# Performance work log

Hardware: AMD Instinct MI355X
Metric: run time of the kernel (lower is better)

The kernel has to match this reference:

```python
import jax, jax.numpy as jnp
import numpy as np

B, C, H, W, K = 16, 512, 64, 64, 64  # K = external-attention latent dim (self.k = 64)


def setup_inputs() -> dict:
    key = jax.random.key(0)
    ks = jax.random.split(key, 5)
    x = jax.random.normal(ks[0], (B, C, H, W), dtype=jnp.float32)
    # conv1: Conv2d(c, c, 1) with bias; init normal(0, sqrt(2/(1*1*out_channels)))
    conv1_w = jax.random.normal(ks[1], (C, C), dtype=jnp.float32) * np.float32(np.sqrt(2.0 / C))
    conv1_b = jnp.zeros((C,), dtype=jnp.float32)
    # linear_0: Conv1d(c, k, 1, bias=False); init normal(0, sqrt(2/out_channels))
    lin0_w = jax.random.normal(ks[2], (K, C), dtype=jnp.float32) * np.float32(np.sqrt(2.0 / K))
    # linear_1: Conv1d(k, c, 1, bias=False)
    lin1_w = jax.random.normal(ks[3], (C, K), dtype=jnp.float32) * np.float32(np.sqrt(2.0 / C))
    # conv2: Conv2d(c, c, 1, bias=False)
    conv2_w = jax.random.normal(ks[4], (C, C), dtype=jnp.float32) * np.float32(np.sqrt(2.0 / C))
    return {"x": x, "conv1_w": conv1_w, "conv1_b": conv1_b,
            "lin0_w": lin0_w, "lin1_w": lin1_w, "conv2_w": conv2_w}


def reference(x, conv1_w, conv1_b, lin0_w, lin1_w, conv2_w):
    b, c, h, w = x.shape
    n = h * w
    idn = x
    # conv1: 1x1 conv == per-pixel GEMM
    y = jnp.einsum('oc,bchw->bohw', conv1_w, x) + conv1_b[None, :, None, None]
    y = y.reshape(b, c, n)
    # external attention: linear_0 -> softmax over tokens -> L1 renorm over latent dim
    attn = jnp.einsum('kc,bcn->bkn', lin0_w, y)          # (b, K, n)
    attn = jax.nn.softmax(attn, axis=-1)
    attn = attn / (1e-9 + attn.sum(axis=1, keepdims=True))
    y = jnp.einsum('ck,bkn->bcn', lin1_w, attn)          # (b, c, n)
    # rank: view(-1, c) row-major (as torch .view does), per-row topk threshold,
    # scale below-threshold by 0.75 and the rest by 1.25; output is detached
    # (torch.tensor(pred, requires_grad=False)) -> stop_gradient
    top_k = c // 2
    flat = y.reshape(-1, c)                               # (b*n, c) row-major chunks
    thr = jax.lax.top_k(flat, top_k)[0][:, -1:]           # k-th largest per row
    scaled = jnp.where(flat < thr, 0.75 * flat, 1.25 * flat)
    yr = jax.lax.stop_gradient(scaled).reshape(b, c, h, w)
    # conv2: 1x1 conv no bias + ReLU, residual add, final ReLU
    out = jax.nn.relu(jnp.einsum('oc,bchw->bohw', conv2_w, yr))
    return jax.nn.relu(out + idn)
```

## Files before the change

kernel.cpp:

```cpp
#include <hip/hip_runtime.h>
#include <stdint.h>

typedef unsigned short u16;
typedef unsigned int u32;
using short8 = __attribute__((ext_vector_type(8))) short;
using f32x4  = __attribute__((ext_vector_type(4))) float;

#define BDIM 16
#define CDIM 512
#define KLAT 64
#define NTOK 4096

__device__ __forceinline__ u16 f2bf(float x) {
  union { float f; u32 u; } a; a.f = x;
  u32 r = a.u + 0x7FFFu + ((a.u >> 16) & 1u);
  return (u16)(r >> 16);
}
__device__ __forceinline__ u32 pack2(float a, float b) {
  return (u32)f2bf(a) | ((u32)f2bf(b) << 16);
}
__device__ __forceinline__ u32 f2key(float x) {
  u32 u = __float_as_uint(x);
  return (u & 0x80000000u) ? ~u : (u | 0x80000000u);
}
__device__ __forceinline__ float keyscale(u32 k_, u32 thr) {
  u32 u = (k_ & 0x80000000u) ? (k_ & 0x7FFFFFFFu) : ~k_;
  float v = __uint_as_float(u);
  return (k_ < thr) ? 0.75f * v : 1.25f * v;
}

__global__ __launch_bounds__(256) void k_setup(
    const float* __restrict__ conv1_w, const float* __restrict__ conv1_b,
    const float* __restrict__ lin0_w,  const float* __restrict__ lin1_w,
    const float* __restrict__ conv2_w,
    u16* __restrict__ w0bf, float* __restrict__ b0,
    u16* __restrict__ lin1bf, u16* __restrict__ cwbf)
{
  const int bid = blockIdx.x;
  const int t = threadIdx.x;
  if (bid < 128) {
    const int kb = bid & 15, cb = bid >> 4;
    const int lane = t & 63;
    int k = kb * 4 + (t >> 6);
    k = __builtin_amdgcn_readfirstlane(k);
    const int c = cb * 64 + lane;
    float acc = 0.f;
    const float* l0 = lin0_w + (size_t)k * CDIM;
    const float* cw = conv1_w + c;
#pragma unroll 4
    for (int o = 0; o < CDIM; ++o)
      acc = fmaf(l0[o], cw[(size_t)o * CDIM], acc);
    w0bf[k * CDIM + c] = f2bf(acc);
  } else if (bid == 128) {
    if (t < KLAT) {
      float acc = 0.f;
      for (int c = 0; c < CDIM; ++c) acc = fmaf(lin0_w[t * CDIM + c], conv1_b[c], acc);
      b0[t] = acc;
    }
  } else if (bid < 193) {
    const int b2 = bid - 129;
    const float4* src = (const float4*)conv2_w;
#pragma unroll
    for (int i = 0; i < 4; ++i) {
      int idx = (b2 * 256 + t) + i * 16384;
      float4 v = src[idx];
      uint2 o;
      o.x = pack2(v.x, v.y);
      o.y = pack2(v.z, v.w);
      *(uint2*)(cwbf + (size_t)idx * 4) = o;
    }
  } else {
    const int b2 = bid - 193;
#pragma unroll
    for (int i = 0; i < 4; ++i) {
      int g = b2 * 1024 + i * 256 + t;
      float4 v0 = *(const float4*)(lin1_w + (size_t)g * 8);
      float4 v1 = *(const float4*)(lin1_w + (size_t)g * 8 + 4);
      uint4 o;
      o.x = pack2(v0.x, v0.y); o.y = pack2(v0.z, v0.w);
      o.z = pack2(v1.x, v1.y); o.w = pack2(v1.z, v1.w);
      *(uint4*)(lin1bf + (size_t)g * 8) = o;
    }
  }
}

__global__ __launch_bounds__(256) void k_xpose(
    const float* __restrict__ x, u16* __restrict__ xbt)
{
  __shared__ float tile[32 * 512];
  const int n0 = blockIdx.x * 512, c0 = blockIdx.y * 32, b = blockIdx.z;
  const int t = threadIdx.x;
#pragma unroll
  for (int i = 0; i < 16; ++i) {
    int f4 = t + i * 256;
    int row = f4 >> 7, col4 = f4 & 127;
    float4 v = *(const float4*)(x + ((size_t)(b * CDIM + c0 + row)) * NTOK + n0 + col4 * 4);
    int phys4 = (col4 + row + (row >> 3)) & 127;
    *(float4*)&tile[row * 512 + phys4 * 4] = v;
  }
  __syncthreads();
#pragma unroll
  for (int i = 0; i < 8; ++i) {
    int nr = (t >> 2) + i * 64;
    int cs = (t & 3) * 8;
    float w[8];
#pragma unroll
    for (int j = 0; j < 8; ++j) {
      int row = cs + j;
      int phys4 = ((nr >> 2) + row + (row >> 3)) & 127;
      w[j] = tile[row * 512 + phys4 * 4 + (nr & 3)];
    }
    uint4 o;
    o.x = pack2(w[0], w[1]); o.y = pack2(w[2], w[3]);
    o.z = pack2(w[4], w[5]); o.w = pack2(w[6], w[7]);
    *(uint4*)(xbt + ((size_t)(b * NTOK + n0 + nr)) * CDIM + c0 + cs) = o;
  }
}

__global__ __launch_bounds__(256) void k_logits(
    const u16* __restrict__ w0bf, const u16* __restrict__ xbt,
    const float* __restrict__ b0, float* __restrict__ logits)
{
  __shared__ u16 As[64 * 72];
  __shared__ u16 Bs[128 * 72];
  const int nb = blockIdx.x, b = blockIdx.y;
  const int t = threadIdx.x;
  const int wv = t >> 6, lane = t & 63;
  const int quad = lane >> 4, l15 = lane & 15;
  f32x4 acc[4][2];
#pragma unroll
  for (int mi = 0; mi < 4; ++mi)
#pragma unroll
    for (int ni = 0; ni < 2; ++ni) acc[mi][ni] = (f32x4){0.f, 0.f, 0.f, 0.f};

  for (int kc = 0; kc < 8; ++kc) {
#pragma unroll
    for (int i = 0; i < 2; ++i) {
      int ch = t + i * 256;
      int row = ch >> 3, col = (ch & 7) * 8;
      uint4 a = *(const uint4*)(w0bf + (size_t)row * CDIM + kc * 64 + col);
      *(uint4*)&As[row * 72 + col] = a;
    }
#pragma unroll
    for (int i = 0; i < 4; ++i) {
      int ch = t + i * 256;
      int row = ch >> 3, col = (ch & 7) * 8;
      uint4 bb = *(const uint4*)(xbt + ((size_t)(b * NTOK + nb * 128 + row)) * CDIM + kc * 64 + col);
      *(uint4*)&Bs[row * 72 + col] = bb;
    }
    __syncthreads();
#pragma unroll
    for (int kk = 0; kk < 2; ++kk) {
      short8 af[4], bf_[2];
#pragma unroll
      for (int mi = 0; mi < 4; ++mi)
        af[mi] = *(short8*)&As[(mi * 16 + l15) * 72 + kk * 32 + quad * 8];
#pragma unroll
      for (int ni = 0; ni < 2; ++ni)
        bf_[ni] = *(short8*)&Bs[(wv * 32 + ni * 16 + l15) * 72 + kk * 32 + quad * 8];
#pragma unroll
      for (int mi = 0; mi < 4; ++mi)
#pragma unroll
        for (int ni = 0; ni < 2; ++ni)
          acc[mi][ni] = __builtin_amdgcn_mfma_f32_16x16x32_bf16(
              af[mi], bf_[ni], acc[mi][ni], 0, 0, 0);
    }
    __syncthreads();
  }
#pragma unroll
  for (int mi = 0; mi < 4; ++mi) {
#pragma unroll
    for (int ni = 0; ni < 2; ++ni) {
#pragma unroll
      for (int r = 0; r < 4; ++r) {
        int row = mi * 16 + quad * 4 + r;
        int col = nb * 128 + wv * 32 + ni * 16 + l15;
        logits[((size_t)(b * KLAT + row)) * NTOK + col] = acc[mi][ni][r] + b0[row];
      }
    }
  }
}

__global__ __launch_bounds__(256) void k_softmax(float* __restrict__ attn)
{
  __shared__ float red[4], red2[4];
  const int t = threadIdx.x;
  float* p = attn + (size_t)blockIdx.x * NTOK;
  float4 v[4];
#pragma unroll
  for (int i = 0; i < 4; ++i) v[i] = ((float4*)p)[t + i * 256];
  float m = v[0].x;
#pragma unroll
  for (int i = 0; i < 4; ++i)
    m = fmaxf(m, fmaxf(fmaxf(v[i].x, v[i].y), fmaxf(v[i].z, v[i].w)));
#pragma unroll
  for (int o = 1; o < 64; o <<= 1) m = fmaxf(m, __shfl_xor(m, o));
  const int wv = t >> 6, lane = t & 63;
  if (lane == 0) red[wv] = m;
  __syncthreads();
  m = fmaxf(fmaxf(red[0], red[1]), fmaxf(red[2], red[3]));
  float s = 0.f;
#pragma unroll
  for (int i = 0; i < 4; ++i) {
    v[i].x = __expf(v[i].x - m); s += v[i].x;
    v[i].y = __expf(v[i].y - m); s += v[i].y;
    v[i].z = __expf(v[i].z - m); s += v[i].z;
    v[i].w = __expf(v[i].w - m); s += v[i].w;
  }
#pragma unroll
  for (int o = 1; o < 64; o <<= 1) s += __shfl_xor(s, o);
  if (lane == 0) red2[wv] = s;
  __syncthreads();
  s = red2[0] + red2[1] + red2[2] + red2[3];
  const float inv = 1.f / s;
#pragma unroll
  for (int i = 0; i < 4; ++i) {
    v[i].x *= inv; v[i].y *= inv; v[i].z *= inv; v[i].w *= inv;
    ((float4*)p)[t + i * 256] = v[i];
  }
}

__global__ __launch_bounds__(256) void k_attnT(
    const float* __restrict__ attn, u16* __restrict__ attnT)
{
  __shared__ float tile[64 * 256];
  __shared__ float inv_[256];
  const int n0 = blockIdx.x * 256, b = blockIdx.y;
  const int t = threadIdx.x;
#pragma unroll
  for (int i = 0; i < 16; ++i) {
    int f4 = t + i * 256;
    int row = f4 >> 6, col4 = f4 & 63;
    float4 v = *(const float4*)(attn + ((size_t)(b * KLAT + row)) * NTOK + n0 + col4 * 4);
    int phys4 = (col4 + row + (row >> 3)) & 63;
    *(float4*)&tile[row * 256 + phys4 * 4] = v;
  }
  __syncthreads();
  {
    int n4 = t >> 2, sub = t & 3;
    float s = 0.f;
#pragma unroll
    for (int k = 0; k < 64; ++k) {
      int phys4 = (n4 + k + (k >> 3)) & 63;
      s += tile[k * 256 + phys4 * 4 + sub];
    }
    inv_[t] = 1.f / (1e-9f + s);
  }
  __syncthreads();
#pragma unroll
  for (int i = 0; i < 8; ++i) {
    int nr = (t >> 3) + i * 32;
    int cs = (t & 7) * 8;
    float sc = inv_[nr];
    float w[8];
#pragma unroll
    for (int j = 0; j < 8; ++j) {
      int row = cs + j;
      int phys4 = ((nr >> 2) + row + (row >> 3)) & 63;
      w[j] = tile[row * 256 + phys4 * 4 + (nr & 3)] * sc;
    }
    uint4 o;
    o.x = pack2(w[0], w[1]); o.y = pack2(w[2], w[3]);
    o.z = pack2(w[4], w[5]); o.w = pack2(w[6], w[7]);
    *(uint4*)(attnT + ((size_t)(b * NTOK + n0 + nr)) * KLAT + cs) = o;
  }
}

__global__ __launch_bounds__(256) void k_lin1rank(
    const u16* __restrict__ lin1bf, const u16* __restrict__ attnT,
    u16* __restrict__ yrt)
{
  __shared__ float tile[32 * 512];
  const int n0 = blockIdx.x * 512, c0 = blockIdx.y * 32, b = blockIdx.z;
  const int t = threadIdx.x;
  const int wv = t >> 6, lane = t & 63;
  const int quad = lane >> 4, l15 = lane & 15;

  short8 af[2][2], bfr[8][2];
#pragma unroll
  for (int mi = 0; mi < 2; ++mi)
#pragma unroll
    for (int kk = 0; kk < 2; ++kk)
      af[mi][kk] = *(const short8*)(lin1bf +
          (size_t)(c0 + mi * 16 + l15) * KLAT + kk * 32 + quad * 8);
#pragma unroll
  for (int ni = 0; ni < 8; ++ni)
#pragma unroll
    for (int kk = 0; kk < 2; ++kk)
      bfr[ni][kk] = *(const short8*)(attnT +
          ((size_t)(b * NTOK + n0 + wv * 128 + ni * 16 + l15)) * KLAT + kk * 32 + quad * 8);
  f32x4 acc[2][8];
#pragma unroll
  for (int mi = 0; mi < 2; ++mi)
#pragma unroll
    for (int ni = 0; ni < 8; ++ni) acc[mi][ni] = (f32x4){0.f, 0.f, 0.f, 0.f};
#pragma unroll
  for (int kk = 0; kk < 2; ++kk)
#pragma unroll
    for (int mi = 0; mi < 2; ++mi)
#pragma unroll
      for (int ni = 0; ni < 8; ++ni)
        acc[mi][ni] = __builtin_amdgcn_mfma_f32_16x16x32_bf16(
            af[mi][kk], bfr[ni][kk], acc[mi][ni], 0, 0, 0);
#pragma unroll
  for (int mi = 0; mi < 2; ++mi) {
#pragma unroll
    for (int ni = 0; ni < 8; ++ni) {
#pragma unroll
      for (int r = 0; r < 4; ++r) {
        int row = mi * 16 + quad * 4 + r;
        int col = wv * 128 + ni * 16 + l15;
        int phys4 = ((col >> 2) + row + (row >> 3)) & 127;
        tile[row * 512 + phys4 * 4 + (col & 3)] = acc[mi][ni][r];
      }
    }
  }
  __syncthreads();

  u32 key[8][8];
#pragma unroll
  for (int r = 0; r < 8; ++r) {
    const int row = wv * 8 + r;
    const int rot = row + (row >> 3);
    const int c4a = (lane + rot) & 127;
    const int c4b = (64 + lane + rot) & 127;
    float4 va = *(const float4*)&tile[row * 512 + c4a * 4];
    float4 vb = *(const float4*)&tile[row * 512 + c4b * 4];
    key[r][0] = f2key(va.x); key[r][1] = f2key(va.y);
    key[r][2] = f2key(va.z); key[r][3] = f2key(va.w);
    key[r][4] = f2key(vb.x); key[r][5] = f2key(vb.y);
    key[r][6] = f2key(vb.z); key[r][7] = f2key(vb.w);
  }
  u32 thr[8] = {0u, 0u, 0u, 0u, 0u, 0u, 0u, 0u};
  for (int bit = 31; bit >= 0; --bit) {
    const u32 m = 1u << bit;
#pragma unroll
    for (int r = 0; r < 8; ++r) {
      u32 cand = thr[r] | m;
      int cnt = 0;
#pragma unroll
      for (int j = 0; j < 8; ++j)
        cnt += (int)__popcll(__ballot(key[r][j] >= cand));
      if (cnt >= 256) thr[r] = cand;
    }
  }
#pragma unroll
  for (int r = 0; r < 8; ++r) {
    const int row = wv * 8 + r;
    const int rot = row + (row >> 3);
    const int c4a = (lane + rot) & 127;
    const int c4b = (64 + lane + rot) & 127;
    float4 oa, ob;
    oa.x = keyscale(key[r][0], thr[r]); oa.y = keyscale(key[r][1], thr[r]);
    oa.z = keyscale(key[r][2], thr[r]); oa.w = keyscale(key[r][3], thr[r]);
    ob.x = keyscale(key[r][4], thr[r]); ob.y = keyscale(key[r][5], thr[r]);
    ob.z = keyscale(key[r][6], thr[r]); ob.w = keyscale(key[r][7], thr[r]);
    *(float4*)&tile[row * 512 + c4a * 4] = oa;
    *(float4*)&tile[row * 512 + c4b * 4] = ob;
  }
  __syncthreads();

#pragma unroll
  for (int i = 0; i < 8; ++i) {
    int nr = (t >> 2) + i * 64;
    int cs = (t & 3) * 8;
    float w[8];
#pragma unroll
    for (int j = 0; j < 8; ++j) {
      int row = cs + j;
      int phys4 = ((nr >> 2) + row + (row >> 3)) & 127;
      w[j] = tile[row * 512 + phys4 * 4 + (nr & 3)];
    }
    uint4 o;
    o.x = pack2(w[0], w[1]); o.y = pack2(w[2], w[3]);
    o.z = pack2(w[4], w[5]); o.w = pack2(w[6], w[7]);
    *(uint4*)(yrt + ((size_t)(b * NTOK + n0 + nr)) * CDIM + c0 + cs) = o;
  }
}

__global__ __launch_bounds__(256) void k_conv2(
    const u16* __restrict__ cwbf, const u16* __restrict__ yrt,
    const float* __restrict__ x, float* __restrict__ out)
{
  __shared__ u16 As[128 * 72];
  __shared__ u16 Bs[128 * 72];
  const int nb = blockIdx.x, mb = blockIdx.y, b = blockIdx.z;
  const int t = threadIdx.x;
  const int wv = t >> 6, lane = t & 63;
  const int wm = wv >> 1, wn = wv & 1;
  const int quad = lane >> 4, l15 = lane & 15;
  f32x4 acc[4][4];
#pragma unroll
  for (int mi = 0; mi < 4; ++mi)
#pragma unroll
    for (int ni = 0; ni < 4; ++ni) acc[mi][ni] = (f32x4){0.f, 0.f, 0.f, 0.f};

  for (int kc = 0; kc < 8; ++kc) {
#pragma unroll
    for (int i = 0; i < 4; ++i) {
      int ch = t + i * 256;
      int row = ch >> 3, col = (ch & 7) * 8;
      uint4 a = *(const uint4*)(cwbf + ((size_t)(mb * 128 + row)) * CDIM + kc * 64 + col);
      *(uint4*)&As[row * 72 + col] = a;
      uint4 bb = *(const uint4*)(yrt + ((size_t)(b * NTOK + nb * 128 + row)) * CDIM + kc * 64 + col);
      *(uint4*)&Bs[row * 72 + col] = bb;
    }
    __syncthreads();
#pragma unroll
    for (int kk = 0; kk < 2; ++kk) {
      short8 af[4], bf_[4];
#pragma unroll
      for (int mi = 0; mi < 4; ++mi)
        af[mi] = *(short8*)&As[(wm * 64 + mi * 16 + l15) * 72 + kk * 32 + quad * 8];
#pragma unroll
      for (int ni = 0; ni < 4; ++ni)
        bf_[ni] = *(short8*)&Bs[(wn * 64 + ni * 16 + l15) * 72 + kk * 32 + quad * 8];
#pragma unroll
      for (int mi = 0; mi < 4; ++mi)
#pragma unroll
        for (int ni = 0; ni < 4; ++ni)
          acc[mi][ni] = __builtin_amdgcn_mfma_f32_16x16x32_bf16(
              af[mi], bf_[ni], acc[mi][ni], 0, 0, 0);
    }
    __syncthreads();
  }
#pragma unroll
  for (int mi = 0; mi < 4; ++mi) {
#pragma unroll
    for (int ni = 0; ni < 4; ++ni) {
#pragma unroll
      for (int r = 0; r < 4; ++r) {
        int row = mb * 128 + wm * 64 + mi * 16 + quad * 4 + r;
        int col = nb * 128 + wn * 64 + ni * 16 + l15;
        size_t off = ((size_t)(b * CDIM + row)) * NTOK + col;
        float g = fmaxf(acc[mi][ni][r], 0.f) + x[off];
        out[off] = fmaxf(g, 0.f);
      }
    }
  }
}

extern "C" void kernel_launch(void* const* d_in, const int* in_sizes, int n_in,
                              void* d_out, int out_size, void* d_ws, size_t ws_size,
                              hipStream_t stream)
{
  const float* x       = (const float*)d_in[0];
  const float* conv1_w = (const float*)d_in[1];
  const float* conv1_b = (const float*)d_in[2];
  const float* lin0_w  = (const float*)d_in[3];
  const float* lin1_w  = (const float*)d_in[4];
  const float* conv2_w = (const float*)d_in[5];
  float* out = (float*)d_out;

  char* ws = (char*)d_ws;
  float* attn  = (float*)ws;
  u16*   xbt   = (u16*)(ws + 16777216);
  u16*   yrt   = xbt;
  u16*   attnT = (u16*)d_out;
  char*  wsm   = ws + 16777216 + 67108864;
  u16*   w0bf  = (u16*)wsm;
  float* b0    = (float*)(wsm + 131072);
  u16*   lin1bf= (u16*)(wsm + 131328);
  u16*   cwbf  = (u16*)(wsm + 262400);

  k_setup   <<<197, 256, 0, stream>>>(conv1_w, conv1_b, lin0_w, lin1_w, conv2_w,
                                      w0bf, b0, lin1bf, cwbf);
  k_xpose   <<<dim3(8, 16, 16), 256, 0, stream>>>(x, xbt);
  k_logits  <<<dim3(32, 16), 256, 0, stream>>>(w0bf, xbt, b0, attn);
  k_softmax <<<1024, 256, 0, stream>>>(attn);
  k_attnT   <<<dim3(16, 16), 256, 0, stream>>>(attn, attnT);
  k_lin1rank<<<dim3(8, 16, 16), 256, 0, stream>>>(lin1bf, attnT, yrt);
  k_conv2   <<<dim3(32, 4, 16), 256, 0, stream>>>(cwbf, yrt, x, out);
}
```

Before: 535.9 us.

## Use value-range bisection for per-row top-k threshold and double block threads

The rank kernel now runs 512 threads per block, so each wave owns 4 rows instead of 8 and the matching slices of the MFMA and writeback work. The fixed 32-step radix bit search for the k-th largest key is replaced by a bisection between the row's min and max keys (found with wave shuffles), which stops early when exactly 256 keys reach the midpoint. This is meant to cut the ballot/popcount iterations spent finding the threshold and to raise parallelism. In exchange the loop length now depends on the data and diverges across rows, and each thread holds fewer accumulators.

```diff
diff --git a/kernel.cpp b/kernel.cpp
--- a/kernel.cpp
+++ b/kernel.cpp
@@ -266,7 +266,7 @@
   }
 }
 
-__global__ __launch_bounds__(256) void k_lin1rank(
+__global__ __launch_bounds__(512) void k_lin1rank(
     const u16* __restrict__ lin1bf, const u16* __restrict__ attnT,
     u16* __restrict__ yrt)
 {
@@ -276,7 +276,7 @@
   const int wv = t >> 6, lane = t & 63;
   const int quad = lane >> 4, l15 = lane & 15;
 
-  short8 af[2][2], bfr[8][2];
+  short8 af[2][2], bfr[4][2];
 #pragma unroll
   for (int mi = 0; mi < 2; ++mi)
 #pragma unroll
@@ -284,32 +284,32 @@
       af[mi][kk] = *(const short8*)(lin1bf +
           (size_t)(c0 + mi * 16 + l15) * KLAT + kk * 32 + quad * 8);
 #pragma unroll
-  for (int ni = 0; ni < 8; ++ni)
+  for (int ni = 0; ni < 4; ++ni)
 #pragma unroll
     for (int kk = 0; kk < 2; ++kk)
       bfr[ni][kk] = *(const short8*)(attnT +
-          ((size_t)(b * NTOK + n0 + wv * 128 + ni * 16 + l15)) * KLAT + kk * 32 + quad * 8);
-  f32x4 acc[2][8];
+          ((size_t)(b * NTOK + n0 + wv * 64 + ni * 16 + l15)) * KLAT + kk * 32 + quad * 8);
+  f32x4 acc[2][4];
 #pragma unroll
   for (int mi = 0; mi < 2; ++mi)
 #pragma unroll
-    for (int ni = 0; ni < 8; ++ni) acc[mi][ni] = (f32x4){0.f, 0.f, 0.f, 0.f};
+    for (int ni = 0; ni < 4; ++ni) acc[mi][ni] = (f32x4){0.f, 0.f, 0.f, 0.f};
 #pragma unroll
   for (int kk = 0; kk < 2; ++kk)
 #pragma unroll
     for (int mi = 0; mi < 2; ++mi)
 #pragma unroll
-      for (int ni = 0; ni < 8; ++ni)
+      for (int ni = 0; ni < 4; ++ni)
         acc[mi][ni] = __builtin_amdgcn_mfma_f32_16x16x32_bf16(
             af[mi][kk], bfr[ni][kk], acc[mi][ni], 0, 0, 0);
 #pragma unroll
   for (int mi = 0; mi < 2; ++mi) {
 #pragma unroll
-    for (int ni = 0; ni < 8; ++ni) {
+    for (int ni = 0; ni < 4; ++ni) {
 #pragma unroll
       for (int r = 0; r < 4; ++r) {
         int row = mi * 16 + quad * 4 + r;
-        int col = wv * 128 + ni * 16 + l15;
+        int col = wv * 64 + ni * 16 + l15;
         int phys4 = ((col >> 2) + row + (row >> 3)) & 127;
         tile[row * 512 + phys4 * 4 + (col & 3)] = acc[mi][ni][r];
       }
@@ -317,52 +317,60 @@
   }
   __syncthreads();
 
-  u32 key[8][8];
-#pragma unroll
-  for (int r = 0; r < 8; ++r) {
-    const int row = wv * 8 + r;
+#pragma unroll
+  for (int r = 0; r < 4; ++r) {
+    const int row = wv * 4 + r;
     const int rot = row + (row >> 3);
     const int c4a = (lane + rot) & 127;
     const int c4b = (64 + lane + rot) & 127;
-    float4 va = *(const float4*)&tile[row * 512 + c4a * 4];
-    float4 vb = *(const float4*)&tile[row * 512 + c4b * 4];
-    key[r][0] = f2key(va.x); key[r][1] = f2key(va.y);
-    key[r][2] = f2key(va.z); key[r][3] = f2key(va.w);
-    key[r][4] = f2key(vb.x); key[r][5] = f2key(vb.y);
-    key[r][6] = f2key(vb.z); key[r][7] = f2key(vb.w);
-  }
-  u32 thr[8] = {0u, 0u, 0u, 0u, 0u, 0u, 0u, 0u};
-  for (int bit = 31; bit >= 0; --bit) {
-    const u32 m = 1u << bit;
-#pragma unroll
-    for (int r = 0; r < 8; ++r) {
-      u32 cand = thr[r] | m;
+    float* pa = &tile[row * 512 + c4a * 4];
+    float* pb = &tile[row * 512 + c4b * 4];
+    float4 va = *(const float4*)pa;
+    float4 vb = *(const float4*)pb;
+    u32 key[8];
+    key[0] = f2key(va.x); key[1] = f2key(va.y);
+    key[2] = f2key(va.z); key[3] = f2key(va.w);
+    key[4] = f2key(vb.x); key[5] = f2key(vb.y);
+    key[6] = f2key(vb.z); key[7] = f2key(vb.w);
+    u32 kmin = key[0], kmax = key[0];
+#pragma unroll
+    for (int j = 1; j < 8; ++j) {
+      kmin = key[j] < kmin ? key[j] : kmin;
+      kmax = key[j] > kmax ? key[j] : kmax;
+    }
+#pragma unroll
+    for (int o = 1; o < 64; o <<= 1) {
+      u32 a_ = __shfl_xor(kmin, o), b_ = __shfl_xor(kmax, o);
+      kmin = a_ < kmin ? a_ : kmin;
+      kmax = b_ > kmax ? b_ : kmax;
+    }
+    u32 lo = kmin, hi = kmax;
+    u32 thr;
+    if (lo >= hi) thr = lo;
+    else for (;;) {
+      u32 d = hi - lo;
+      u32 mid = lo + (d >> 1) + (d & 1u);
       int cnt = 0;
 #pragma unroll
       for (int j = 0; j < 8; ++j)
-        cnt += (int)__popcll(__ballot(key[r][j] >= cand));
-      if (cnt >= 256) thr[r] = cand;
-    }
-  }
-#pragma unroll
-  for (int r = 0; r < 8; ++r) {
-    const int row = wv * 8 + r;
-    const int rot = row + (row >> 3);
-    const int c4a = (lane + rot) & 127;
-    const int c4b = (64 + lane + rot) & 127;
+        cnt += (int)__popcll(__ballot(key[j] >= mid));
+      if (cnt == 256) { thr = mid; break; }
+      if (cnt > 256) lo = mid; else hi = mid - 1u;
+      if (lo >= hi) { thr = lo; break; }
+    }
     float4 oa, ob;
-    oa.x = keyscale(key[r][0], thr[r]); oa.y = keyscale(key[r][1], thr[r]);
-    oa.z = keyscale(key[r][2], thr[r]); oa.w = keyscale(key[r][3], thr[r]);
-    ob.x = keyscale(key[r][4], thr[r]); ob.y = keyscale(key[r][5], thr[r]);
-    ob.z = keyscale(key[r][6], thr[r]); ob.w = keyscale(key[r][7], thr[r]);
-    *(float4*)&tile[row * 512 + c4a * 4] = oa;
-    *(float4*)&tile[row * 512 + c4b * 4] = ob;
-  }
-  __syncthreads();
-
-#pragma unroll
-  for (int i = 0; i < 8; ++i) {
-    int nr = (t >> 2) + i * 64;
+    oa.x = keyscale(key[0], thr); oa.y = keyscale(key[1], thr);
+    oa.z = keyscale(key[2], thr); oa.w = keyscale(key[3], thr);
+    ob.x = keyscale(key[4], thr); ob.y = keyscale(key[5], thr);
+    ob.z = keyscale(key[6], thr); ob.w = keyscale(key[7], thr);
+    *(float4*)pa = oa;
+    *(float4*)pb = ob;
+  }
+  __syncthreads();
+
+#pragma unroll
+  for (int i = 0; i < 4; ++i) {
+    int nr = (t >> 2) + i * 128;
     int cs = (t & 3) * 8;
     float w[8];
 #pragma unroll
@@ -469,6 +477,6 @@
   k_logits  <<<dim3(32, 16), 256, 0, stream>>>(w0bf, xbt, b0, attn);
   k_softmax <<<1024, 256, 0, stream>>>(attn);
   k_attnT   <<<dim3(16, 16), 256, 0, stream>>>(attn, attnT);
-  k_lin1rank<<<dim3(8, 16, 16), 256, 0, stream>>>(lin1bf, attnT, yrt);
+  k_lin1rank<<<dim3(8, 16, 16), 512, 0, stream>>>(lin1bf, attnT, yrt);
   k_conv2   <<<dim3(32, 4, 16), 256, 0, stream>>>(cwbf, yrt, x, out);
 }
```

After: 486.3 us. -9.3%, faster.

## Fuse x transpose into logits GEMM, widen rank kernel, range-bisect top-k threshold

Applied to the files above, without the earlier changes.

Removes the standalone transpose/bf16 conversion kernel. The logits GEMM now loads fp32 x directly into a swizzled shared tile and converts to bf16 while building MFMA fragments, which saves a full write and read of the bf16 transposed copy. The lin1+rank kernel moves to 512 threads so each wave handles 4 rows instead of 8. Its per-row k-th-largest search changes from a fixed 32-bit radix walk to a bisection over the row's min..max key range that stops early on an exact count. In exchange there are more LDS reads and conversions inside the GEMM inner loop, and the bisection has a data-dependent iteration count.

```diff
diff --git a/kernel.cpp b/kernel.cpp
--- a/kernel.cpp
+++ b/kernel.cpp
@@ -84,45 +84,12 @@
   }
 }
 
-__global__ __launch_bounds__(256) void k_xpose(
-    const float* __restrict__ x, u16* __restrict__ xbt)
-{
-  __shared__ float tile[32 * 512];
-  const int n0 = blockIdx.x * 512, c0 = blockIdx.y * 32, b = blockIdx.z;
-  const int t = threadIdx.x;
-#pragma unroll
-  for (int i = 0; i < 16; ++i) {
-    int f4 = t + i * 256;
-    int row = f4 >> 7, col4 = f4 & 127;
-    float4 v = *(const float4*)(x + ((size_t)(b * CDIM + c0 + row)) * NTOK + n0 + col4 * 4);
-    int phys4 = (col4 + row + (row >> 3)) & 127;
-    *(float4*)&tile[row * 512 + phys4 * 4] = v;
-  }
-  __syncthreads();
-#pragma unroll
-  for (int i = 0; i < 8; ++i) {
-    int nr = (t >> 2) + i * 64;
-    int cs = (t & 3) * 8;
-    float w[8];
-#pragma unroll
-    for (int j = 0; j < 8; ++j) {
-      int row = cs + j;
-      int phys4 = ((nr >> 2) + row + (row >> 3)) & 127;
-      w[j] = tile[row * 512 + phys4 * 4 + (nr & 3)];
-    }
-    uint4 o;
-    o.x = pack2(w[0], w[1]); o.y = pack2(w[2], w[3]);
-    o.z = pack2(w[4], w[5]); o.w = pack2(w[6], w[7]);
-    *(uint4*)(xbt + ((size_t)(b * NTOK + n0 + nr)) * CDIM + c0 + cs) = o;
-  }
-}
-
 __global__ __launch_bounds__(256) void k_logits(
-    const u16* __restrict__ w0bf, const u16* __restrict__ xbt,
+    const u16* __restrict__ w0bf, const float* __restrict__ x,
     const float* __restrict__ b0, float* __restrict__ logits)
 {
   __shared__ u16 As[64 * 72];
-  __shared__ u16 Bs[128 * 72];
+  __shared__ float xt[64 * 128];
   const int nb = blockIdx.x, b = blockIdx.y;
   const int t = threadIdx.x;
   const int wv = t >> 6, lane = t & 63;
@@ -142,11 +109,13 @@
       *(uint4*)&As[row * 72 + col] = a;
     }
 #pragma unroll
-    for (int i = 0; i < 4; ++i) {
-      int ch = t + i * 256;
-      int row = ch >> 3, col = (ch & 7) * 8;
-      uint4 bb = *(const uint4*)(xbt + ((size_t)(b * NTOK + nb * 128 + row)) * CDIM + kc * 64 + col);
-      *(uint4*)&Bs[row * 72 + col] = bb;
+    for (int i = 0; i < 8; ++i) {
+      int f4 = t + i * 256;
+      int row = f4 >> 5, col4 = f4 & 31;
+      float4 v = *(const float4*)(x + ((size_t)(b * CDIM + kc * 64 + row)) * NTOK
+                                  + nb * 128 + col4 * 4);
+      int phys4 = (col4 + row + (row >> 3)) & 31;
+      *(float4*)&xt[row * 128 + phys4 * 4] = v;
     }
     __syncthreads();
 #pragma unroll
@@ -156,8 +125,20 @@
       for (int mi = 0; mi < 4; ++mi)
         af[mi] = *(short8*)&As[(mi * 16 + l15) * 72 + kk * 32 + quad * 8];
 #pragma unroll
-      for (int ni = 0; ni < 2; ++ni)
-        bf_[ni] = *(short8*)&Bs[(wv * 32 + ni * 16 + l15) * 72 + kk * 32 + quad * 8];
+      for (int ni = 0; ni < 2; ++ni) {
+        const int n = wv * 32 + ni * 16 + l15;
+        const int n4 = n >> 2, ns = n & 3;
+        union { u32 u[4]; short8 s; } cvt;
+#pragma unroll
+        for (int jj = 0; jj < 4; ++jj) {
+          int ca = kk * 32 + quad * 8 + jj * 2;
+          int cb2 = ca + 1;
+          float v0 = xt[ca * 128 + (((n4 + ca + (ca >> 3)) & 31) * 4) + ns];
+          float v1 = xt[cb2 * 128 + (((n4 + cb2 + (cb2 >> 3)) & 31) * 4) + ns];
+          cvt.u[jj] = pack2(v0, v1);
+        }
+        bf_[ni] = cvt.s;
+      }
 #pragma unroll
       for (int mi = 0; mi < 4; ++mi)
 #pragma unroll
@@ -266,7 +247,7 @@
   }
 }
 
-__global__ __launch_bounds__(256) void k_lin1rank(
+__global__ __launch_bounds__(512) void k_lin1rank(
     const u16* __restrict__ lin1bf, const u16* __restrict__ attnT,
     u16* __restrict__ yrt)
 {
@@ -276,7 +257,7 @@
   const int wv = t >> 6, lane = t & 63;
   const int quad = lane >> 4, l15 = lane & 15;
 
-  short8 af[2][2], bfr[8][2];
+  short8 af[2][2], bfr[4][2];
 #pragma unroll
   for (int mi = 0; mi < 2; ++mi)
 #pragma unroll
@@ -284,32 +265,32 @@
       af[mi][kk] = *(const short8*)(lin1bf +
           (size_t)(c0 + mi * 16 + l15) * KLAT + kk * 32 + quad * 8);
 #pragma unroll
-  for (int ni = 0; ni < 8; ++ni)
+  for (int ni = 0; ni < 4; ++ni)
 #pragma unroll
     for (int kk = 0; kk < 2; ++kk)
       bfr[ni][kk] = *(const short8*)(attnT +
-          ((size_t)(b * NTOK + n0 + wv * 128 + ni * 16 + l15)) * KLAT + kk * 32 + quad * 8);
-  f32x4 acc[2][8];
+          ((size_t)(b * NTOK + n0 + wv * 64 + ni * 16 + l15)) * KLAT + kk * 32 + quad * 8);
+  f32x4 acc[2][4];
 #pragma unroll
   for (int mi = 0; mi < 2; ++mi)
 #pragma unroll
-    for (int ni = 0; ni < 8; ++ni) acc[mi][ni] = (f32x4){0.f, 0.f, 0.f, 0.f};
+    for (int ni = 0; ni < 4; ++ni) acc[mi][ni] = (f32x4){0.f, 0.f, 0.f, 0.f};
 #pragma unroll
   for (int kk = 0; kk < 2; ++kk)
 #pragma unroll
     for (int mi = 0; mi < 2; ++mi)
 #pragma unroll
-      for (int ni = 0; ni < 8; ++ni)
+      for (int ni = 0; ni < 4; ++ni)
         acc[mi][ni] = __builtin_amdgcn_mfma_f32_16x16x32_bf16(
             af[mi][kk], bfr[ni][kk], acc[mi][ni], 0, 0, 0);
 #pragma unroll
   for (int mi = 0; mi < 2; ++mi) {
 #pragma unroll
-    for (int ni = 0; ni < 8; ++ni) {
+    for (int ni = 0; ni < 4; ++ni) {
 #pragma unroll
       for (int r = 0; r < 4; ++r) {
         int row = mi * 16 + quad * 4 + r;
-        int col = wv * 128 + ni * 16 + l15;
+        int col = wv * 64 + ni * 16 + l15;
         int phys4 = ((col >> 2) + row + (row >> 3)) & 127;
         tile[row * 512 + phys4 * 4 + (col & 3)] = acc[mi][ni][r];
       }
@@ -317,10 +298,10 @@
   }
   __syncthreads();
 
-  u32 key[8][8];
-#pragma unroll
-  for (int r = 0; r < 8; ++r) {
-    const int row = wv * 8 + r;
+  u32 key[4][8];
+#pragma unroll
+  for (int r = 0; r < 4; ++r) {
+    const int row = wv * 4 + r;
     const int rot = row + (row >> 3);
     const int c4a = (lane + rot) & 127;
     const int c4b = (64 + lane + rot) & 127;
@@ -331,22 +312,70 @@
     key[r][4] = f2key(vb.x); key[r][5] = f2key(vb.y);
     key[r][6] = f2key(vb.z); key[r][7] = f2key(vb.w);
   }
-  u32 thr[8] = {0u, 0u, 0u, 0u, 0u, 0u, 0u, 0u};
-  for (int bit = 31; bit >= 0; --bit) {
-    const u32 m = 1u << bit;
-#pragma unroll
-    for (int r = 0; r < 8; ++r) {
-      u32 cand = thr[r] | m;
-      int cnt = 0;
-#pragma unroll
-      for (int j = 0; j < 8; ++j)
-        cnt += (int)__popcll(__ballot(key[r][j] >= cand));
-      if (cnt >= 256) thr[r] = cand;
-    }
-  }
-#pragma unroll
-  for (int r = 0; r < 8; ++r) {
-    const int row = wv * 8 + r;
+  u32 lo[4], hi[4];
+#pragma unroll
+  for (int r = 0; r < 4; ++r) {
+    u32 kmin = key[r][0], kmax = key[r][0];
+#pragma unroll
+    for (int j = 1; j < 8; ++j) {
+      kmin = key[r][j] < kmin ? key[r][j] : kmin;
+      kmax = key[r][j] > kmax ? key[r][j] : kmax;
+    }
+    lo[r] = kmin; hi[r] = kmax;
+  }
+#pragma unroll
+  for (int o = 1; o < 64; o <<= 1) {
+#pragma unroll
+    for (int r = 0; r < 4; ++r) {
+      u32 a_ = __shfl_xor(lo[r], o), b_ = __shfl_xor(hi[r], o);
+      lo[r] = a_ < lo[r] ? a_ : lo[r];
+      hi[r] = b_ > hi[r] ? b_ : hi[r];
+    }
+  }
+  u32 thr[4];
+  bool done[4];
+#pragma unroll
+  for (int r = 0; r < 4; ++r) {
+    thr[r] = lo[r];
+    done[r] = (lo[r] >= hi[r]);
+  }
+  for (int it = 0; it < 33; ++it) {
+    bool any = false;
+    u32 mid[4];
+#pragma unroll
+    for (int r = 0; r < 4; ++r) {
+      if (!done[r]) {
+        any = true;
+        u32 d = hi[r] - lo[r];
+        mid[r] = lo[r] + (d >> 1) + (d & 1u);
+      }
+    }
+    if (!any) break;
+    int cnt[4];
+#pragma unroll
+    for (int r = 0; r < 4; ++r) {
+      if (!done[r]) {
+        int c = 0;
+#pragma unroll
+        for (int j = 0; j < 8; ++j)
+          c += (int)__popcll(__ballot(key[r][j] >= mid[r]));
+        cnt[r] = c;
+      }
+    }
+#pragma unroll
+    for (int r = 0; r < 4; ++r) {
+      if (!done[r]) {
+        if (cnt[r] == 256) { thr[r] = mid[r]; done[r] = true; }
+        else {
+          if (cnt[r] > 256) lo[r] = mid[r]; else hi[r] = mid[r] - 1u;
+          if (lo[r] >= hi[r]) { thr[r] = lo[r]; done[r] = true; }
+        }
+      }
+    }
+  }
+#pragma unroll
+  for (int r = 0; r < 4; ++r) {
+    const int row = wv * 4 + r;
     const int rot = row + (row >> 3);
     const int c4a = (lane + rot) & 127;
     const int c4b = (64 + lane + rot) & 127;
@@ -361,8 +390,8 @@
   __syncthreads();
 
 #pragma unroll
-  for (int i = 0; i < 8; ++i) {
-    int nr = (t >> 2) + i * 64;
+  for (int i = 0; i < 4; ++i) {
+    int nr = (t >> 2) + i * 128;
     int cs = (t & 3) * 8;
     float w[8];
 #pragma unroll
@@ -454,8 +483,7 @@
 
   char* ws = (char*)d_ws;
   float* attn  = (float*)ws;
-  u16*   xbt   = (u16*)(ws + 16777216);
-  u16*   yrt   = xbt;
+  u16*   yrt   = (u16*)(ws + 16777216);
   u16*   attnT = (u16*)d_out;
   char*  wsm   = ws + 16777216 + 67108864;
   u16*   w0bf  = (u16*)wsm;
@@ -465,10 +493,9 @@
 
   k_setup   <<<197, 256, 0, stream>>>(conv1_w, conv1_b, lin0_w, lin1_w, conv2_w,
                                       w0bf, b0, lin1bf, cwbf);
-  k_xpose   <<<dim3(8, 16, 16), 256, 0, stream>>>(x, xbt);
-  k_logits  <<<dim3(32, 16), 256, 0, stream>>>(w0bf, xbt, b0, attn);
+  k_logits  <<<dim3(32, 16), 256, 0, stream>>>(w0bf, x, b0, attn);
   k_softmax <<<1024, 256, 0, stream>>>(attn);
   k_attnT   <<<dim3(16, 16), 256, 0, stream>>>(attn, attnT);
-  k_lin1rank<<<dim3(8, 16, 16), 256, 0, stream>>>(lin1bf, attnT, yrt);
+  k_lin1rank<<<dim3(8, 16, 16), 512, 0, stream>>>(lin1bf, attnT, yrt);
   k_conv2   <<<dim3(32, 4, 16), 256, 0, stream>>>(cwbf, yrt, x, out);
 }
```

Result: faster. 503.8 us (-6.0%).
